# Kernel optimization log

Hardware: AMD Instinct MI355X
Metric: run time of the kernel (lower is better)

Reference implementation:

```python
import jax, jax.numpy as jnp
import numpy as np

B, S, D = 4, 2048, 1024
H = 16
HD = D // H  # head_dim = key_dim = value_dim = 64


def setup_inputs() -> dict:
    key = jax.random.key(0)
    ks = jax.random.split(key, 4)
    scale = (2.0 / (D + D)) ** 0.5  # xavier_normal for square weight
    return {
        "hidden_states": jax.random.normal(ks[0], (B, S, D), dtype=jnp.float32),
        "Wq": jax.random.normal(ks[1], (D, D), dtype=jnp.float32) * scale,
        "bq": jnp.zeros((D,), dtype=jnp.float32),
        "Wk": jax.random.normal(ks[2], (D, D), dtype=jnp.float32) * scale,
        "bk": jnp.zeros((D,), dtype=jnp.float32),
        "Wv": jax.random.normal(ks[3], (D, D), dtype=jnp.float32) * scale,
        "bv": jnp.zeros((D,), dtype=jnp.float32),
    }


def _split_heads(x):
    # [B, S, H*HD] -> [B, H, S, HD]
    b, s, _ = x.shape
    return x.reshape(b, s, H, HD).transpose(0, 2, 1, 3)


def reference(hidden_states, Wq, bq, Wk, bk, Wv, bv):
    # Linear projections (torch Linear: x @ W.T + b)
    q = _split_heads(hidden_states @ Wq.T + bq)  # [B,H,S,HD]
    k = _split_heads(hidden_states @ Wk.T + bk)
    v = _split_heads(hidden_states @ Wv.T + bv)
    scores = jnp.einsum("bhqd,bhkd->bhqk", q, k) / jnp.sqrt(jnp.float32(HD))
    probs = jax.nn.softmax(scores, axis=-1)
    out = jnp.einsum("bhqk,bhkd->bhqd", probs, v)  # [B,H,S,HD]
    # merge heads -> [B, S, H*HD]
    return out.transpose(0, 2, 1, 3).reshape(B, S, H * HD)
```

## Files before the change

### kernel.cpp

```cpp
#include <hip/hip_runtime.h>
#include <math.h>

#define SB 4
#define SS 2048
#define SD 1024
#define SH 16
#define SHD 64
#define SM (SB * SS)

using f32x4 = __attribute__((ext_vector_type(4))) float;
using h8    = __attribute__((ext_vector_type(8))) _Float16;
using h4    = __attribute__((ext_vector_type(4))) _Float16;
using fp16x2 = __fp16 __attribute__((ext_vector_type(2)));
using fp16x4 = __fp16 __attribute__((ext_vector_type(4)));

__device__ __forceinline__ unsigned short f2h(float x) {
  _Float16 h = (_Float16)x;
  return __builtin_bit_cast(unsigned short, h);
}

__device__ __forceinline__ void gld_lds16(const unsigned short* g, unsigned short* l) {
  __builtin_amdgcn_global_load_lds(
      (const __attribute__((address_space(1))) unsigned int*)g,
      (__attribute__((address_space(3))) unsigned int*)l, 16, 0, 0);
}

__global__ __launch_bounds__(256) void cvt4h(const float* __restrict__ in,
                                             unsigned short* __restrict__ out, int n4) {
  int i = blockIdx.x * 256 + threadIdx.x;
  if (i >= n4) return;
  float4 v = ((const float4*)in)[i];
  unsigned long long r = (unsigned long long)f2h(v.x)
                       | ((unsigned long long)f2h(v.y) << 16)
                       | ((unsigned long long)f2h(v.z) << 32)
                       | ((unsigned long long)f2h(v.w) << 48);
  ((unsigned long long*)out)[i] = r;
}

__global__ __launch_bounds__(256) void cvt3w(const float* __restrict__ w0, const float* __restrict__ w1,
                                             const float* __restrict__ w2,
                                             unsigned short* __restrict__ o0, unsigned short* __restrict__ o1,
                                             unsigned short* __restrict__ o2) {
  const int z = blockIdx.y;
  const float* in = (z == 0) ? w0 : (z == 1) ? w1 : w2;
  unsigned short* out = (z == 0) ? o0 : (z == 1) ? o1 : o2;
  int i = blockIdx.x * 256 + threadIdx.x;
  float4 v = ((const float4*)in)[i];
  unsigned long long r = (unsigned long long)f2h(v.x)
                       | ((unsigned long long)f2h(v.y) << 16)
                       | ((unsigned long long)f2h(v.z) << 32)
                       | ((unsigned long long)f2h(v.w) << 48);
  ((unsigned long long*)out)[i] = r;
}

__global__ __launch_bounds__(256) void gemm_qkv(
    const unsigned short* __restrict__ Xh,
    const unsigned short* __restrict__ Wqh, const unsigned short* __restrict__ Wkh,
    const unsigned short* __restrict__ Wvh,
    const float* __restrict__ bq, const float* __restrict__ bk, const float* __restrict__ bv,
    unsigned short* __restrict__ Qh, unsigned short* __restrict__ Kh,
    unsigned short* __restrict__ Vt) {
  __shared__ unsigned short lA[128 * 64];
  __shared__ unsigned short lB[128 * 64];
  const int L = blockIdx.x;
  const int xcd = L & 7, rr = L >> 3;
  const int mloc = rr & 7, widx = rr >> 3;
  const int tNi = widx & 7, z = widx >> 3;
  const int tM = (xcd * 8 + mloc) * 128, tN = tNi * 128;

  const unsigned short* W = (z == 0) ? Wqh : (z == 1) ? Wkh : Wvh;
  const float* bias = (z == 0) ? bq : (z == 1) ? bk : bv;

  const int tid = threadIdx.x;
  const int wave = tid >> 6, lane = tid & 63;
  const int quad = lane >> 4, l16 = lane & 15;
  const int wr = (wave >> 1) * 64, wc = (wave & 1) * 64;

  f32x4 acc[4][4] = {};

  const int rB = tid >> 3;
  const int colOff = (((tid & 7) ^ (rB & 7))) * 8;
  const unsigned short* gA[4];
  const unsigned short* gB[4];
#pragma unroll
  for (int i = 0; i < 4; ++i) {
    gA[i] = Xh + (size_t)(tM + i * 32 + rB) * SD + colOff;
    gB[i] = W  + (size_t)(tN + i * 32 + rB) * SD + colOff;
  }
  unsigned short* dA[4];
  unsigned short* dB[4];
#pragma unroll
  for (int i = 0; i < 4; ++i) {
    dA[i] = lA + (i * 256 + wave * 64) * 8;
    dB[i] = lB + (i * 256 + wave * 64) * 8;
  }
  const int swl = l16 & 7;

  if (z == 2) {
    for (int k0 = 0; k0 < SD; k0 += 64) {
      __syncthreads();
#pragma unroll
      for (int i = 0; i < 4; ++i) gld_lds16(gA[i] + k0, dA[i]);
#pragma unroll
      for (int i = 0; i < 4; ++i) gld_lds16(gB[i] + k0, dB[i]);
      __syncthreads();
#pragma unroll
      for (int ks = 0; ks < 2; ++ks) {
        h8 af[4], bf[4];
#pragma unroll
        for (int mi = 0; mi < 4; ++mi)
          af[mi] = *(const h8*)(lA + (wr + mi * 16 + l16) * 64 + (((ks * 4 + quad) ^ swl) * 8));
#pragma unroll
        for (int ni = 0; ni < 4; ++ni)
          bf[ni] = *(const h8*)(lB + (wc + ni * 16 + l16) * 64 + (((ks * 4 + quad) ^ swl) * 8));
#pragma unroll
        for (int mi = 0; mi < 4; ++mi)
#pragma unroll
          for (int ni = 0; ni < 4; ++ni)
            acc[mi][ni] = __builtin_amdgcn_mfma_f32_16x16x32_f16(af[mi], bf[ni], acc[mi][ni], 0, 0, 0);
      }
    }
#pragma unroll
    for (int ni = 0; ni < 4; ++ni) {
      const int gn = tN + wc + ni * 16 + l16;
      const float bb = bias[gn];
#pragma unroll
      for (int mi = 0; mi < 4; ++mi) {
        const int gm = tM + wr + mi * 16 + quad * 4;
        const int vb = gm >> 11, vs = gm & 2047;
        unsigned long long wv = 0;
#pragma unroll
        for (int r = 0; r < 4; ++r)
          wv |= (unsigned long long)f2h(acc[mi][ni][r] + bb) << (16 * r);
        *(unsigned long long*)(Vt + (size_t)(vb * 1024 + gn) * SS + vs) = wv;
      }
    }
  } else {
    for (int k0 = 0; k0 < SD; k0 += 64) {
      __syncthreads();
#pragma unroll
      for (int i = 0; i < 4; ++i) gld_lds16(gA[i] + k0, dA[i]);
#pragma unroll
      for (int i = 0; i < 4; ++i) gld_lds16(gB[i] + k0, dB[i]);
      __syncthreads();
#pragma unroll
      for (int ks = 0; ks < 2; ++ks) {
        h8 af[4], bf[4];
#pragma unroll
        for (int mi = 0; mi < 4; ++mi)
          af[mi] = *(const h8*)(lA + (wr + mi * 16 + l16) * 64 + (((ks * 4 + quad) ^ swl) * 8));
#pragma unroll
        for (int ni = 0; ni < 4; ++ni)
          bf[ni] = *(const h8*)(lB + (wc + ni * 16 + l16) * 64 + (((ks * 4 + quad) ^ swl) * 8));
#pragma unroll
        for (int mi = 0; mi < 4; ++mi)
#pragma unroll
          for (int ni = 0; ni < 4; ++ni)
            acc[mi][ni] = __builtin_amdgcn_mfma_f32_16x16x32_f16(bf[ni], af[mi], acc[mi][ni], 0, 0, 0);
      }
    }
    const float sc = (z == 0) ? 0.18033688011112042f : 1.0f;
    unsigned short* C = (z == 0) ? Qh : Kh;
#pragma unroll
    for (int mi = 0; mi < 4; ++mi) {
      const int gm = tM + wr + mi * 16 + l16;
#pragma unroll
      for (int ni = 0; ni < 4; ++ni) {
        const int gnb = tN + wc + ni * 16 + quad * 4;
        const float4 bb4 = *(const float4*)(bias + gnb);
        unsigned long long wv;
        wv  = (unsigned long long)f2h((acc[mi][ni][0] + bb4.x) * sc);
        wv |= (unsigned long long)f2h((acc[mi][ni][1] + bb4.y) * sc) << 16;
        wv |= (unsigned long long)f2h((acc[mi][ni][2] + bb4.z) * sc) << 32;
        wv |= (unsigned long long)f2h((acc[mi][ni][3] + bb4.w) * sc) << 48;
        *(unsigned long long*)(C + (size_t)gm * SD + gnb) = wv;
      }
    }
  }
}

__global__ __launch_bounds__(256, 4) void attn(const unsigned short* __restrict__ Qh,
                                               const unsigned short* __restrict__ Kh,
                                               const unsigned short* __restrict__ Vt,
                                               float* __restrict__ out) {
  __shared__ unsigned short lK[2][64 * 64];
  __shared__ unsigned short lV[2][64 * 64];
  __shared__ unsigned short pl[4 * 16 * 64];
  const int tid = threadIdx.x;
  const int wave = tid >> 6, lane = tid & 63;
  const int quad = lane >> 4, l16 = lane & 15;
  const int qh = quad >> 1, ql = quad & 1;
  const int bid = blockIdx.x;
  const int bh = (bid & 7) | (((bid >> 3) & 7) << 3);
  const int qt = bid >> 6;
  const int b = bh >> 4, h = bh & 15;
  const int qsA = qt * 128 + wave * 16;

  const unsigned short* qpA = Qh + ((size_t)(b * SS + qsA + l16)) * SD + h * 64 + quad * 8;
  const unsigned short* qpB = qpA + (size_t)64 * SD;
  h8 aqA0 = *(const h8*)(qpA);
  h8 aqA1 = *(const h8*)(qpA + 32);
  h8 aqB0 = *(const h8*)(qpB);
  h8 aqB1 = *(const h8*)(qpB + 32);

  const int row0 = tid >> 3, cs0 = (tid & 7) ^ (row0 & 7);
  const int row1 = row0 + 32, cs1 = (tid & 7) ^ (row1 & 7);
  const unsigned short* kS0 = Kh + ((size_t)(b * SS + row0)) * SD + h * 64 + cs0 * 8;
  const unsigned short* kS1 = Kh + ((size_t)(b * SS + row1)) * SD + h * 64 + cs1 * 8;
  const unsigned short* vS0 = Vt + ((size_t)(bh * 64 + row0)) * SS + cs0 * 8;
  const unsigned short* vS1 = Vt + ((size_t)(bh * 64 + row1)) * SS + cs1 * 8;
  unsigned short* dK0 = &lK[0][wave * 512];
  unsigned short* dK1 = &lK[0][2048 + wave * 512];
  unsigned short* dV0 = &lV[0][wave * 512];
  unsigned short* dV1 = &lV[0][2048 + wave * 512];

  f32x4 ovA[4] = {}, ovB[4] = {};
  float l_accA = 0.f, l_accB = 0.f;
  const int swl = l16 & 7;
  unsigned short* plw = pl + wave * 1024;
  unsigned short* pwr = plw + l16 * 64;
  unsigned short* pwrW = pwr + ql * 4;

  gld_lds16(kS0, dK0); gld_lds16(kS1, dK1);
  gld_lds16(vS0, dV0); gld_lds16(vS1, dV1);
  kS0 += 64 * SD; kS1 += 64 * SD; vS0 += 64; vS1 += 64;

  for (int kt = 0; kt < 32; ++kt) {
    const int buf = kt & 1;
    __syncthreads();
    if (kt < 31) {
      const int o = (buf ^ 1) * 64 * 64;
      gld_lds16(kS0, dK0 + o); gld_lds16(kS1, dK1 + o);
      gld_lds16(vS0, dV0 + o); gld_lds16(vS1, dV1 + o);
      kS0 += 64 * SD; kS1 += 64 * SD; vS0 += 64; vS1 += 64;
    }
    const unsigned short* Kt = lK[buf];
    const unsigned short* Vl = lV[buf];

    f32x4 sA[4], sB[4];
#pragma unroll
    for (int nt = 0; nt < 4; ++nt) {
      const unsigned short* kr = Kt + (nt * 16 + l16) * 64;
      h8 kf0 = *(const h8*)(kr + ((quad ^ swl) * 8));
      h8 kf1 = *(const h8*)(kr + (((4 + quad) ^ swl) * 8));
      f32x4 zA = {};
      zA = __builtin_amdgcn_mfma_f32_16x16x32_f16(kf0, aqA0, zA, 0, 0, 0);
      sA[nt] = __builtin_amdgcn_mfma_f32_16x16x32_f16(kf1, aqA1, zA, 0, 0, 0);
      f32x4 zB = {};
      zB = __builtin_amdgcn_mfma_f32_16x16x32_f16(kf0, aqB0, zB, 0, 0, 0);
      sB[nt] = __builtin_amdgcn_mfma_f32_16x16x32_f16(kf1, aqB1, zB, 0, 0, 0);
    }

#pragma unroll
    for (int g = 0; g < 4; ++g) {
      float p0 = __builtin_amdgcn_exp2f(sA[g][0]);
      float p1 = __builtin_amdgcn_exp2f(sA[g][1]);
      float p2 = __builtin_amdgcn_exp2f(sA[g][2]);
      float p3 = __builtin_amdgcn_exp2f(sA[g][3]);
      l_accA += (p0 + p1) + (p2 + p3);
      fp16x2 lo = __builtin_amdgcn_cvt_pkrtz(p0, p1);
      fp16x2 hi = __builtin_amdgcn_cvt_pkrtz(p2, p3);
      fp16x4 pk = __builtin_shufflevector(lo, hi, 0, 1, 2, 3);
      *(unsigned long long*)(pwrW + ((2 * g + qh) ^ swl) * 8) =
          __builtin_bit_cast(unsigned long long, pk);
    }
    asm volatile("s_waitcnt lgkmcnt(0)" ::: "memory");
    h8 pbA0 = *(const h8*)(pwr + ((quad ^ swl) * 8));
    h8 pbA1 = *(const h8*)(pwr + (((4 + quad) ^ swl) * 8));

#pragma unroll
    for (int g = 0; g < 4; ++g) {
      float p0 = __builtin_amdgcn_exp2f(sB[g][0]);
      float p1 = __builtin_amdgcn_exp2f(sB[g][1]);
      float p2 = __builtin_amdgcn_exp2f(sB[g][2]);
      float p3 = __builtin_amdgcn_exp2f(sB[g][3]);
      l_accB += (p0 + p1) + (p2 + p3);
      fp16x2 lo = __builtin_amdgcn_cvt_pkrtz(p0, p1);
      fp16x2 hi = __builtin_amdgcn_cvt_pkrtz(p2, p3);
      fp16x4 pk = __builtin_shufflevector(lo, hi, 0, 1, 2, 3);
      *(unsigned long long*)(pwrW + ((2 * g + qh) ^ swl) * 8) =
          __builtin_bit_cast(unsigned long long, pk);
    }
    asm volatile("s_waitcnt lgkmcnt(0)" ::: "memory");
    h8 pbB0 = *(const h8*)(pwr + ((quad ^ swl) * 8));
    h8 pbB1 = *(const h8*)(pwr + (((4 + quad) ^ swl) * 8));

#pragma unroll
    for (int f = 0; f < 4; ++f) {
      const unsigned short* vr = Vl + (f * 16 + l16) * 64;
      h8 v0 = *(const h8*)(vr + ((quad ^ swl) * 8));
      h8 v1 = *(const h8*)(vr + (((4 + quad) ^ swl) * 8));
      ovA[f] = __builtin_amdgcn_mfma_f32_16x16x32_f16(v0, pbA0, ovA[f], 0, 0, 0);
      ovA[f] = __builtin_amdgcn_mfma_f32_16x16x32_f16(v1, pbA1, ovA[f], 0, 0, 0);
      ovB[f] = __builtin_amdgcn_mfma_f32_16x16x32_f16(v0, pbB0, ovB[f], 0, 0, 0);
      ovB[f] = __builtin_amdgcn_mfma_f32_16x16x32_f16(v1, pbB1, ovB[f], 0, 0, 0);
    }
  }
  float ltA = l_accA;
  ltA += __shfl_xor(ltA, 16);
  ltA += __shfl_xor(ltA, 32);
  const float invA = 1.0f / ltA;
  float ltB = l_accB;
  ltB += __shfl_xor(ltB, 16);
  ltB += __shfl_xor(ltB, 32);
  const float invB = 1.0f / ltB;
  float* orowA = out + ((size_t)(b * SS + qsA + l16)) * SD + h * 64 + quad * 4;
  float* orowB = orowA + (size_t)64 * SD;
#pragma unroll
  for (int f = 0; f < 4; ++f) {
    float4 w;
    w.x = ovA[f][0] * invA; w.y = ovA[f][1] * invA;
    w.z = ovA[f][2] * invA; w.w = ovA[f][3] * invA;
    *(float4*)(orowA + f * 16) = w;
    float4 u;
    u.x = ovB[f][0] * invB; u.y = ovB[f][1] * invB;
    u.z = ovB[f][2] * invB; u.w = ovB[f][3] * invB;
    *(float4*)(orowB + f * 16) = u;
  }
}

extern "C" void kernel_launch(void* const* d_in, const int* in_sizes, int n_in,
                              void* d_out, int out_size, void* d_ws, size_t ws_size,
                              hipStream_t stream) {
  const float* hs = (const float*)d_in[0];
  const float* Wq = (const float*)d_in[1];
  const float* bq = (const float*)d_in[2];
  const float* Wk = (const float*)d_in[3];
  const float* bk = (const float*)d_in[4];
  const float* Wv = (const float*)d_in[5];
  const float* bv = (const float*)d_in[6];
  float* out = (float*)d_out;

  char* ws = (char*)d_ws;
  unsigned short* Xh  = (unsigned short*)(ws);
  unsigned short* Wqh = (unsigned short*)(ws + 16777216);
  unsigned short* Wkh = (unsigned short*)(ws + 16777216 + 2097152);
  unsigned short* Wvh = (unsigned short*)(ws + 16777216 + 2 * 2097152);
  unsigned short* Qh  = (unsigned short*)(ws + 16777216 + 3 * 2097152);
  unsigned short* Kh  = Qh + (size_t)SM * SD;
  unsigned short* Vt  = Kh + (size_t)SM * SD;

  cvt4h<<<dim3(8192), dim3(256), 0, stream>>>(hs, Xh, SM * SD / 4);
  cvt3w<<<dim3(1024, 3), dim3(256), 0, stream>>>(Wq, Wk, Wv, Wqh, Wkh, Wvh);
  gemm_qkv<<<dim3(1536), dim3(256), 0, stream>>>(
      Xh, Wqh, Wkh, Wvh, bq, bk, bv, Qh, Kh, Vt);
  attn<<<dim3(SB * SH * (SS / 128)), dim3(256), 0, stream>>>(Qh, Kh, Vt, out);
}
```

Before: 251.3 us.

## Replace LDS round-trip for P with permlane32 swaps and permuted V loads

```diff
diff --git a/kernel.cpp b/kernel.cpp
--- a/kernel.cpp
+++ b/kernel.cpp
@@ -13,6 +13,8 @@
 using h4    = __attribute__((ext_vector_type(4))) _Float16;
 using fp16x2 = __fp16 __attribute__((ext_vector_type(2)));
 using fp16x4 = __fp16 __attribute__((ext_vector_type(4)));
+using u32x4 = __attribute__((ext_vector_type(4))) unsigned int;
+using u64x2 = __attribute__((ext_vector_type(2))) unsigned long long;
 
 __device__ __forceinline__ unsigned short f2h(float x) {
   _Float16 h = (_Float16)x;
@@ -185,11 +187,9 @@
                                                float* __restrict__ out) {
   __shared__ unsigned short lK[2][64 * 64];
   __shared__ unsigned short lV[2][64 * 64];
-  __shared__ unsigned short pl[4 * 16 * 64];
   const int tid = threadIdx.x;
   const int wave = tid >> 6, lane = tid & 63;
   const int quad = lane >> 4, l16 = lane & 15;
-  const int qh = quad >> 1, ql = quad & 1;
   const int bid = blockIdx.x;
   const int bh = (bid & 7) | (((bid >> 3) & 7) << 3);
   const int qt = bid >> 6;
@@ -216,10 +216,13 @@
 
   f32x4 ovA[4] = {}, ovB[4] = {};
   float l_accA = 0.f, l_accB = 0.f;
-  const int swl = l16 & 7;
-  unsigned short* plw = pl + wave * 1024;
-  unsigned short* pwr = plw + l16 * 64;
-  unsigned short* pwrW = pwr + ql * 4;
+  const int swl = l16 & 15 & 7;
+  const int Q2 = quad >> 1, hq = quad & 1;
+  const int ko0 = (quad ^ swl) * 8, ko1 = ((4 + quad) ^ swl) * 8;
+  const int vo0 = ((2 * Q2) ^ swl) * 8 + hq * 4;
+  const int vo1 = ((2 * Q2 + 1) ^ swl) * 8 + hq * 4;
+  const int vo2 = ((4 + 2 * Q2) ^ swl) * 8 + hq * 4;
+  const int vo3 = ((5 + 2 * Q2) ^ swl) * 8 + hq * 4;
 
   gld_lds16(kS0, dK0); gld_lds16(kS1, dK1);
   gld_lds16(vS0, dV0); gld_lds16(vS1, dV1);
@@ -241,8 +244,8 @@
 #pragma unroll
     for (int nt = 0; nt < 4; ++nt) {
       const unsigned short* kr = Kt + (nt * 16 + l16) * 64;
-      h8 kf0 = *(const h8*)(kr + ((quad ^ swl) * 8));
-      h8 kf1 = *(const h8*)(kr + (((4 + quad) ^ swl) * 8));
+      h8 kf0 = *(const h8*)(kr + ko0);
+      h8 kf1 = *(const h8*)(kr + ko1);
       f32x4 zA = {};
       zA = __builtin_amdgcn_mfma_f32_16x16x32_f16(kf0, aqA0, zA, 0, 0, 0);
       sA[nt] = __builtin_amdgcn_mfma_f32_16x16x32_f16(kf1, aqA1, zA, 0, 0, 0);
@@ -251,6 +254,7 @@
       sB[nt] = __builtin_amdgcn_mfma_f32_16x16x32_f16(kf1, aqB1, zB, 0, 0, 0);
     }
 
+    unsigned ulA[4], uhA[4];
 #pragma unroll
     for (int g = 0; g < 4; ++g) {
       float p0 = __builtin_amdgcn_exp2f(sA[g][0]);
@@ -258,16 +262,19 @@
       float p2 = __builtin_amdgcn_exp2f(sA[g][2]);
       float p3 = __builtin_amdgcn_exp2f(sA[g][3]);
       l_accA += (p0 + p1) + (p2 + p3);
-      fp16x2 lo = __builtin_amdgcn_cvt_pkrtz(p0, p1);
-      fp16x2 hi = __builtin_amdgcn_cvt_pkrtz(p2, p3);
-      fp16x4 pk = __builtin_shufflevector(lo, hi, 0, 1, 2, 3);
-      *(unsigned long long*)(pwrW + ((2 * g + qh) ^ swl) * 8) =
-          __builtin_bit_cast(unsigned long long, pk);
-    }
-    asm volatile("s_waitcnt lgkmcnt(0)" ::: "memory");
-    h8 pbA0 = *(const h8*)(pwr + ((quad ^ swl) * 8));
-    h8 pbA1 = *(const h8*)(pwr + (((4 + quad) ^ swl) * 8));
-
+      ulA[g] = __builtin_bit_cast(unsigned, __builtin_amdgcn_cvt_pkrtz(p0, p1));
+      uhA[g] = __builtin_bit_cast(unsigned, __builtin_amdgcn_cvt_pkrtz(p2, p3));
+    }
+    auto aA0 = __builtin_amdgcn_permlane32_swap(ulA[0], ulA[1], false, false);
+    auto aA1 = __builtin_amdgcn_permlane32_swap(uhA[0], uhA[1], false, false);
+    auto aA2 = __builtin_amdgcn_permlane32_swap(ulA[2], ulA[3], false, false);
+    auto aA3 = __builtin_amdgcn_permlane32_swap(uhA[2], uhA[3], false, false);
+    u32x4 wA0 = {aA0[0], aA1[0], aA0[1], aA1[1]};
+    u32x4 wA1 = {aA2[0], aA3[0], aA2[1], aA3[1]};
+    h8 pbA0 = __builtin_bit_cast(h8, wA0);
+    h8 pbA1 = __builtin_bit_cast(h8, wA1);
+
+    unsigned ulB[4], uhB[4];
 #pragma unroll
     for (int g = 0; g < 4; ++g) {
       float p0 = __builtin_amdgcn_exp2f(sB[g][0]);
@@ -275,21 +282,27 @@
       float p2 = __builtin_amdgcn_exp2f(sB[g][2]);
       float p3 = __builtin_amdgcn_exp2f(sB[g][3]);
       l_accB += (p0 + p1) + (p2 + p3);
-      fp16x2 lo = __builtin_amdgcn_cvt_pkrtz(p0, p1);
-      fp16x2 hi = __builtin_amdgcn_cvt_pkrtz(p2, p3);
-      fp16x4 pk = __builtin_shufflevector(lo, hi, 0, 1, 2, 3);
-      *(unsigned long long*)(pwrW + ((2 * g + qh) ^ swl) * 8) =
-          __builtin_bit_cast(unsigned long long, pk);
-    }
-    asm volatile("s_waitcnt lgkmcnt(0)" ::: "memory");
-    h8 pbB0 = *(const h8*)(pwr + ((quad ^ swl) * 8));
-    h8 pbB1 = *(const h8*)(pwr + (((4 + quad) ^ swl) * 8));
+      ulB[g] = __builtin_bit_cast(unsigned, __builtin_amdgcn_cvt_pkrtz(p0, p1));
+      uhB[g] = __builtin_bit_cast(unsigned, __builtin_amdgcn_cvt_pkrtz(p2, p3));
+    }
+    auto aB0 = __builtin_amdgcn_permlane32_swap(ulB[0], ulB[1], false, false);
+    auto aB1 = __builtin_amdgcn_permlane32_swap(uhB[0], uhB[1], false, false);
+    auto aB2 = __builtin_amdgcn_permlane32_swap(ulB[2], ulB[3], false, false);
+    auto aB3 = __builtin_amdgcn_permlane32_swap(uhB[2], uhB[3], false, false);
+    u32x4 wB0 = {aB0[0], aB1[0], aB0[1], aB1[1]};
+    u32x4 wB1 = {aB2[0], aB3[0], aB2[1], aB3[1]};
+    h8 pbB0 = __builtin_bit_cast(h8, wB0);
+    h8 pbB1 = __builtin_bit_cast(h8, wB1);
 
 #pragma unroll
     for (int f = 0; f < 4; ++f) {
       const unsigned short* vr = Vl + (f * 16 + l16) * 64;
-      h8 v0 = *(const h8*)(vr + ((quad ^ swl) * 8));
-      h8 v1 = *(const h8*)(vr + (((4 + quad) ^ swl) * 8));
+      u64x2 tva = { *(const unsigned long long*)(vr + vo0),
+                    *(const unsigned long long*)(vr + vo1) };
+      u64x2 tvb = { *(const unsigned long long*)(vr + vo2),
+                    *(const unsigned long long*)(vr + vo3) };
+      h8 v0 = __builtin_bit_cast(h8, tva);
+      h8 v1 = __builtin_bit_cast(h8, tvb);
       ovA[f] = __builtin_amdgcn_mfma_f32_16x16x32_f16(v0, pbA0, ovA[f], 0, 0, 0);
       ovA[f] = __builtin_amdgcn_mfma_f32_16x16x32_f16(v1, pbA1, ovA[f], 0, 0, 0);
       ovB[f] = __builtin_amdgcn_mfma_f32_16x16x32_f16(v0, pbB0, ovB[f], 0, 0, 0);
```

New measurement: 250.0 us. Within noise of the previous version (-0.5%).

## Process four query tiles per wave and transpose P via permlane swaps

Applied to the files above, without the earlier changes.

```diff
diff --git a/kernel.cpp b/kernel.cpp
--- a/kernel.cpp
+++ b/kernel.cpp
@@ -13,6 +13,7 @@
 using h4    = __attribute__((ext_vector_type(4))) _Float16;
 using fp16x2 = __fp16 __attribute__((ext_vector_type(2)));
 using fp16x4 = __fp16 __attribute__((ext_vector_type(4)));
+using u32x4 = __attribute__((ext_vector_type(4))) unsigned int;
 
 __device__ __forceinline__ unsigned short f2h(float x) {
   _Float16 h = (_Float16)x;
@@ -179,29 +180,27 @@
   }
 }
 
-__global__ __launch_bounds__(256, 4) void attn(const unsigned short* __restrict__ Qh,
+__global__ __launch_bounds__(256, 2) void attn(const unsigned short* __restrict__ Qh,
                                                const unsigned short* __restrict__ Kh,
                                                const unsigned short* __restrict__ Vt,
                                                float* __restrict__ out) {
   __shared__ unsigned short lK[2][64 * 64];
   __shared__ unsigned short lV[2][64 * 64];
-  __shared__ unsigned short pl[4 * 16 * 64];
   const int tid = threadIdx.x;
   const int wave = tid >> 6, lane = tid & 63;
   const int quad = lane >> 4, l16 = lane & 15;
-  const int qh = quad >> 1, ql = quad & 1;
   const int bid = blockIdx.x;
-  const int bh = (bid & 7) | (((bid >> 3) & 7) << 3);
-  const int qt = bid >> 6;
+  const int bh = bid & 63, qt = bid >> 6;
   const int b = bh >> 4, h = bh & 15;
-  const int qsA = qt * 128 + wave * 16;
-
-  const unsigned short* qpA = Qh + ((size_t)(b * SS + qsA + l16)) * SD + h * 64 + quad * 8;
-  const unsigned short* qpB = qpA + (size_t)64 * SD;
-  h8 aqA0 = *(const h8*)(qpA);
-  h8 aqA1 = *(const h8*)(qpA + 32);
-  h8 aqB0 = *(const h8*)(qpB);
-  h8 aqB1 = *(const h8*)(qpB + 32);
+  const int qs = qt * 256 + wave * 16;
+
+  const unsigned short* qp0 = Qh + ((size_t)(b * SS + qs + l16)) * SD + h * 64 + quad * 8;
+  h8 aq[4][2];
+#pragma unroll
+  for (int x = 0; x < 4; ++x) {
+    aq[x][0] = *(const h8*)(qp0 + (size_t)(x * 64) * SD);
+    aq[x][1] = *(const h8*)(qp0 + (size_t)(x * 64) * SD + 32);
+  }
 
   const int row0 = tid >> 3, cs0 = (tid & 7) ^ (row0 & 7);
   const int row1 = row0 + 32, cs1 = (tid & 7) ^ (row1 & 7);
@@ -214,12 +213,10 @@
   unsigned short* dV0 = &lV[0][wave * 512];
   unsigned short* dV1 = &lV[0][2048 + wave * 512];
 
-  f32x4 ovA[4] = {}, ovB[4] = {};
-  float l_accA = 0.f, l_accB = 0.f;
+  f32x4 ov[4][4] = {};
+  float lacc[4] = {0.f, 0.f, 0.f, 0.f};
   const int swl = l16 & 7;
-  unsigned short* plw = pl + wave * 1024;
-  unsigned short* pwr = plw + l16 * 64;
-  unsigned short* pwrW = pwr + ql * 4;
+  const int ko0 = (quad ^ swl) * 8, ko1 = ((4 + quad) ^ swl) * 8;
 
   gld_lds16(kS0, dK0); gld_lds16(kS1, dK1);
   gld_lds16(vS0, dV0); gld_lds16(vS1, dV1);
@@ -237,85 +234,77 @@
     const unsigned short* Kt = lK[buf];
     const unsigned short* Vl = lV[buf];
 
-    f32x4 sA[4], sB[4];
+    f32x4 s[4][4];
 #pragma unroll
     for (int nt = 0; nt < 4; ++nt) {
       const unsigned short* kr = Kt + (nt * 16 + l16) * 64;
-      h8 kf0 = *(const h8*)(kr + ((quad ^ swl) * 8));
-      h8 kf1 = *(const h8*)(kr + (((4 + quad) ^ swl) * 8));
-      f32x4 zA = {};
-      zA = __builtin_amdgcn_mfma_f32_16x16x32_f16(kf0, aqA0, zA, 0, 0, 0);
-      sA[nt] = __builtin_amdgcn_mfma_f32_16x16x32_f16(kf1, aqA1, zA, 0, 0, 0);
-      f32x4 zB = {};
-      zB = __builtin_amdgcn_mfma_f32_16x16x32_f16(kf0, aqB0, zB, 0, 0, 0);
-      sB[nt] = __builtin_amdgcn_mfma_f32_16x16x32_f16(kf1, aqB1, zB, 0, 0, 0);
-    }
-
-#pragma unroll
-    for (int g = 0; g < 4; ++g) {
-      float p0 = __builtin_amdgcn_exp2f(sA[g][0]);
-      float p1 = __builtin_amdgcn_exp2f(sA[g][1]);
-      float p2 = __builtin_amdgcn_exp2f(sA[g][2]);
-      float p3 = __builtin_amdgcn_exp2f(sA[g][3]);
-      l_accA += (p0 + p1) + (p2 + p3);
-      fp16x2 lo = __builtin_amdgcn_cvt_pkrtz(p0, p1);
-      fp16x2 hi = __builtin_amdgcn_cvt_pkrtz(p2, p3);
-      fp16x4 pk = __builtin_shufflevector(lo, hi, 0, 1, 2, 3);
-      *(unsigned long long*)(pwrW + ((2 * g + qh) ^ swl) * 8) =
-          __builtin_bit_cast(unsigned long long, pk);
-    }
-    asm volatile("s_waitcnt lgkmcnt(0)" ::: "memory");
-    h8 pbA0 = *(const h8*)(pwr + ((quad ^ swl) * 8));
-    h8 pbA1 = *(const h8*)(pwr + (((4 + quad) ^ swl) * 8));
-
-#pragma unroll
-    for (int g = 0; g < 4; ++g) {
-      float p0 = __builtin_amdgcn_exp2f(sB[g][0]);
-      float p1 = __builtin_amdgcn_exp2f(sB[g][1]);
-      float p2 = __builtin_amdgcn_exp2f(sB[g][2]);
-      float p3 = __builtin_amdgcn_exp2f(sB[g][3]);
-      l_accB += (p0 + p1) + (p2 + p3);
-      fp16x2 lo = __builtin_amdgcn_cvt_pkrtz(p0, p1);
-      fp16x2 hi = __builtin_amdgcn_cvt_pkrtz(p2, p3);
-      fp16x4 pk = __builtin_shufflevector(lo, hi, 0, 1, 2, 3);
-      *(unsigned long long*)(pwrW + ((2 * g + qh) ^ swl) * 8) =
-          __builtin_bit_cast(unsigned long long, pk);
-    }
-    asm volatile("s_waitcnt lgkmcnt(0)" ::: "memory");
-    h8 pbB0 = *(const h8*)(pwr + ((quad ^ swl) * 8));
-    h8 pbB1 = *(const h8*)(pwr + (((4 + quad) ^ swl) * 8));
+      h8 kf0 = *(const h8*)(kr + ko0);
+      h8 kf1 = *(const h8*)(kr + ko1);
+#pragma unroll
+      for (int x = 0; x < 4; ++x) {
+        f32x4 z = {};
+        z = __builtin_amdgcn_mfma_f32_16x16x32_f16(kf0, aq[x][0], z, 0, 0, 0);
+        s[x][nt] = __builtin_amdgcn_mfma_f32_16x16x32_f16(kf1, aq[x][1], z, 0, 0, 0);
+      }
+    }
+
+    h8 pb[4][2];
+#pragma unroll
+    for (int x = 0; x < 4; ++x) {
+      unsigned ul[4], uh[4];
+      float la = 0.f;
+#pragma unroll
+      for (int g = 0; g < 4; ++g) {
+        float p0 = __builtin_amdgcn_exp2f(s[x][g][0]);
+        float p1 = __builtin_amdgcn_exp2f(s[x][g][1]);
+        float p2 = __builtin_amdgcn_exp2f(s[x][g][2]);
+        float p3 = __builtin_amdgcn_exp2f(s[x][g][3]);
+        la += (p0 + p1) + (p2 + p3);
+        ul[g] = __builtin_bit_cast(unsigned, __builtin_amdgcn_cvt_pkrtz(p0, p1));
+        uh[g] = __builtin_bit_cast(unsigned, __builtin_amdgcn_cvt_pkrtz(p2, p3));
+      }
+      lacc[x] += la;
+      auto sl0 = __builtin_amdgcn_permlane32_swap(ul[0], ul[1], false, false);
+      auto tl0 = __builtin_amdgcn_permlane16_swap(sl0[0], sl0[1], false, false);
+      auto sh0 = __builtin_amdgcn_permlane32_swap(uh[0], uh[1], false, false);
+      auto th0 = __builtin_amdgcn_permlane16_swap(sh0[0], sh0[1], false, false);
+      u32x4 w0 = {tl0[0], th0[0], tl0[1], th0[1]};
+      pb[x][0] = __builtin_bit_cast(h8, w0);
+      auto sl1 = __builtin_amdgcn_permlane32_swap(ul[2], ul[3], false, false);
+      auto tl1 = __builtin_amdgcn_permlane16_swap(sl1[0], sl1[1], false, false);
+      auto sh1 = __builtin_amdgcn_permlane32_swap(uh[2], uh[3], false, false);
+      auto th1 = __builtin_amdgcn_permlane16_swap(sh1[0], sh1[1], false, false);
+      u32x4 w1 = {tl1[0], th1[0], tl1[1], th1[1]};
+      pb[x][1] = __builtin_bit_cast(h8, w1);
+    }
 
 #pragma unroll
     for (int f = 0; f < 4; ++f) {
       const unsigned short* vr = Vl + (f * 16 + l16) * 64;
-      h8 v0 = *(const h8*)(vr + ((quad ^ swl) * 8));
-      h8 v1 = *(const h8*)(vr + (((4 + quad) ^ swl) * 8));
-      ovA[f] = __builtin_amdgcn_mfma_f32_16x16x32_f16(v0, pbA0, ovA[f], 0, 0, 0);
-      ovA[f] = __builtin_amdgcn_mfma_f32_16x16x32_f16(v1, pbA1, ovA[f], 0, 0, 0);
-      ovB[f] = __builtin_amdgcn_mfma_f32_16x16x32_f16(v0, pbB0, ovB[f], 0, 0, 0);
-      ovB[f] = __builtin_amdgcn_mfma_f32_16x16x32_f16(v1, pbB1, ovB[f], 0, 0, 0);
-    }
-  }
-  float ltA = l_accA;
-  ltA += __shfl_xor(ltA, 16);
-  ltA += __shfl_xor(ltA, 32);
-  const float invA = 1.0f / ltA;
-  float ltB = l_accB;
-  ltB += __shfl_xor(ltB, 16);
-  ltB += __shfl_xor(ltB, 32);
-  const float invB = 1.0f / ltB;
-  float* orowA = out + ((size_t)(b * SS + qsA + l16)) * SD + h * 64 + quad * 4;
-  float* orowB = orowA + (size_t)64 * SD;
-#pragma unroll
-  for (int f = 0; f < 4; ++f) {
-    float4 w;
-    w.x = ovA[f][0] * invA; w.y = ovA[f][1] * invA;
-    w.z = ovA[f][2] * invA; w.w = ovA[f][3] * invA;
-    *(float4*)(orowA + f * 16) = w;
-    float4 u;
-    u.x = ovB[f][0] * invB; u.y = ovB[f][1] * invB;
-    u.z = ovB[f][2] * invB; u.w = ovB[f][3] * invB;
-    *(float4*)(orowB + f * 16) = u;
+      h8 v0 = *(const h8*)(vr + ko0);
+      h8 v1 = *(const h8*)(vr + ko1);
+#pragma unroll
+      for (int x = 0; x < 4; ++x) {
+        ov[x][f] = __builtin_amdgcn_mfma_f32_16x16x32_f16(v0, pb[x][0], ov[x][f], 0, 0, 0);
+        ov[x][f] = __builtin_amdgcn_mfma_f32_16x16x32_f16(v1, pb[x][1], ov[x][f], 0, 0, 0);
+      }
+    }
+  }
+
+#pragma unroll
+  for (int x = 0; x < 4; ++x) {
+    float lt = lacc[x];
+    lt += __shfl_xor(lt, 16);
+    lt += __shfl_xor(lt, 32);
+    const float inv = 1.0f / lt;
+    float* orow = out + ((size_t)(b * SS + qs + x * 64 + l16)) * SD + h * 64 + quad * 4;
+#pragma unroll
+    for (int f = 0; f < 4; ++f) {
+      float4 w;
+      w.x = ov[x][f][0] * inv; w.y = ov[x][f][1] * inv;
+      w.z = ov[x][f][2] * inv; w.w = ov[x][f][3] * inv;
+      *(float4*)(orow + f * 16) = w;
+    }
   }
 }
 
@@ -344,5 +333,5 @@
   cvt3w<<<dim3(1024, 3), dim3(256), 0, stream>>>(Wq, Wk, Wv, Wqh, Wkh, Wvh);
   gemm_qkv<<<dim3(1536), dim3(256), 0, stream>>>(
       Xh, Wqh, Wkh, Wvh, bq, bk, bv, Qh, Kh, Vt);
-  attn<<<dim3(SB * SH * (SS / 128)), dim3(256), 0, stream>>>(Qh, Kh, Vt, out);
-}
+  attn<<<dim3(SB * SH * (SS / 256)), dim3(256), 0, stream>>>(Qh, Kh, Vt, out);
+}
```

Measured after the change: 237.6 us. -5.4%, faster.
